# Optimization experiments

Measured on AMD Instinct MI355X. Metric: run time of the kernel, lower is better.

The kernel has to match this reference:

```python
import jax, jax.numpy as jnp
import numpy as np

NUM_NODES = 1_000_000
N = 100_000      # nodes in sampled subgraph (n_id)
E = 1_000_000    # edges from LastNeighborLoader
TE = 1_500_000   # total stored temporal events
B = 20_000       # batch of (src, dst, neg_dst) events
MEM = 128        # memory_dim
TD = 64          # time_dim
MSG = 64         # raw_msg_dim
EMB = 128        # embedding_dim
H = 2            # TransformerConv heads (out = heads * emb//2)
D = EMB // H
HID = 128        # MLP hidden
OUT = 64         # MLP out / link predictor in_channels
EDGE_DIM = MSG + TD


def setup_inputs() -> dict:
    key = jax.random.key(0)
    ks = iter(jax.random.split(key, 40))
    nrm = lambda shp, s: jax.random.normal(next(ks), shp, dtype=jnp.float32) * s
    inp = {
        'memory_table': nrm((NUM_NODES, MEM), 1.0),
        'last_update_table': jax.random.uniform(next(ks), (NUM_NODES,), dtype=jnp.float32) * 1000.0,
        'graph_t': jax.random.uniform(next(ks), (TE,), dtype=jnp.float32) * 1000.0,
        'graph_msg': nrm((TE, MSG), 1.0),
        'Wt': nrm((1, TD), 1.0), 'bt': nrm((TD,), 1.0),
        'Wq': nrm((MEM, EMB), MEM ** -0.5), 'bq': jnp.zeros((EMB,), jnp.float32),
        'Wk': nrm((MEM, EMB), MEM ** -0.5), 'bk': jnp.zeros((EMB,), jnp.float32),
        'Wv': nrm((MEM, EMB), MEM ** -0.5), 'bv': jnp.zeros((EMB,), jnp.float32),
        'We': nrm((EDGE_DIM, EMB), EDGE_DIM ** -0.5),
        'Wskip': nrm((MEM, EMB), MEM ** -0.5), 'bskip': jnp.zeros((EMB,), jnp.float32),
        'W1': nrm((EMB, HID), EMB ** -0.5), 'b1': jnp.zeros((HID,), jnp.float32),
        'bn_gamma': jnp.ones((HID,), jnp.float32), 'bn_beta': jnp.zeros((HID,), jnp.float32),
        'W2': nrm((HID, OUT), HID ** -0.5), 'b2': jnp.zeros((OUT,), jnp.float32),
        'Wls': nrm((OUT, OUT), OUT ** -0.5), 'bls': jnp.zeros((OUT,), jnp.float32),
        'Wld': nrm((OUT, OUT), OUT ** -0.5), 'bld': jnp.zeros((OUT,), jnp.float32),
        'Wlf': nrm((OUT, 1), OUT ** -0.5), 'blf': jnp.zeros((1,), jnp.float32),
        'n_id': jax.random.randint(next(ks), (N,), 0, NUM_NODES, dtype=jnp.int64) if jax.config.jax_enable_x64 else jax.random.randint(next(ks), (N,), 0, NUM_NODES).astype(jnp.int32),
        'edge_index': jax.random.randint(next(ks), (2, E), 0, N).astype(jnp.int32),
        'e_id': jax.random.randint(next(ks), (E,), 0, TE).astype(jnp.int32),
        'src_idx': jax.random.randint(next(ks), (B,), 0, N).astype(jnp.int32),
        'dst_idx': jax.random.randint(next(ks), (B,), 0, N).astype(jnp.int32),
        'neg_idx': jax.random.randint(next(ks), (B,), 0, N).astype(jnp.int32),
    }
    return inp


def _forward(memory_table, last_update_table, graph_t, graph_msg,
             Wt, bt, Wq, bq, Wk, bk, Wv, bv, We, Wskip, bskip,
             W1, b1, bn_gamma, bn_beta, W2, b2,
             Wls, bls, Wld, bld, Wlf, blf,
             n_id, edge_index, e_id, src_idx, dst_idx, neg_idx):
    # --- memory lookup (TGNMemory.forward for n_id) ---
    x = memory_table[n_id]          # [N, MEM]
    lu = last_update_table[n_id]    # [N]
    src, dst = edge_index[0], edge_index[1]

    # --- temporal edge features ---
    t_e = graph_t[e_id]             # [E]
    msg_e = graph_msg[e_id]         # [E, MSG]
    rel_t = lu[src] - t_e           # [E]
    rel_t_enc = jnp.cos(rel_t[:, None] * Wt[0] + bt)          # TimeEncoder: cos(Linear(1, TD))
    edge_attr = jnp.concatenate([rel_t_enc, msg_e], axis=-1)  # [E, EDGE_DIM]

    # --- TransformerConv (heads=H, head_dim=D, edge_dim) ---
    q = (x @ Wq + bq).reshape(N, H, D)
    k = (x @ Wk + bk).reshape(N, H, D)
    v = (x @ Wv + bv).reshape(N, H, D)
    e_proj = (edge_attr @ We).reshape(E, H, D)
    k_e = k[src] + e_proj
    v_e = v[src] + e_proj
    logits = jnp.einsum('ehd,ehd->eh', q[dst], k_e) / jnp.sqrt(jnp.float32(D))  # [E, H]
    m = jax.ops.segment_max(logits, dst, num_segments=N)      # per-dst max, [N, H]
    w = jnp.exp(logits - m[dst])
    s = jax.ops.segment_sum(w, dst, num_segments=N)           # [N, H]
    alpha = w / (s[dst] + 1e-16)                               # softmax over incoming edges
    agg = jax.ops.segment_sum(alpha[..., None] * v_e, dst, num_segments=N)  # [N, H, D]
    z = agg.reshape(N, EMB) + (x @ Wskip + bskip)              # root/skip connection

    # --- MLP([EMB, HID, OUT]) with batch_norm + relu between layers ---
    h = z @ W1 + b1
    mu = jnp.mean(h, axis=0)
    var = jnp.mean(jnp.square(h - mu), axis=0)
    h = (h - mu) * jax.lax.rsqrt(var + 1e-5) * bn_gamma + bn_beta
    h = jax.nn.relu(h)
    z2 = h @ W2 + b2                                           # [N, OUT]

    # --- link prediction on assoc-gathered embeddings ---
    z_src, z_dst, z_neg = z2[src_idx], z2[dst_idx], z2[neg_idx]

    def link_pred(a, b):
        hh = jax.nn.relu(a @ Wls + bls + b @ Wld + bld)
        return hh @ Wlf + blf                                  # [B, 1]

    return link_pred(z_src, z_dst), link_pred(z_src, z_neg)


def reference(memory_table, last_update_table, graph_t, graph_msg,
              Wt, bt, Wq, bq, Wk, bk, Wv, bv, We, Wskip, bskip,
              W1, b1, bn_gamma, bn_beta, W2, b2,
              Wls, bls, Wld, bld, Wlf, blf,
              n_id, edge_index, e_id, src_idx, dst_idx, neg_idx):
    return _forward(memory_table, last_update_table, graph_t, graph_msg,
                    Wt, bt, Wq, bq, Wk, bk, Wv, bv, We, Wskip, bskip,
                    W1, b1, bn_gamma, bn_beta, W2, b2,
                    Wls, bls, Wld, bld, Wlf, blf,
                    n_id, edge_index, e_id, src_idx, dst_idx, neg_idx)
```

## Files before the change

### kernel.cpp

```cpp
#include <hip/hip_runtime.h>

#define NN 100000
#define EE 1000000
#define BB 20000
#define NB 100352
#define NCH 98

__global__ __launch_bounds__(256) void k_hist(
    const int* __restrict__ eidx, int* __restrict__ bins)
{
    int e = blockIdx.x * 256 + threadIdx.x;
    if (e < EE) atomicAdd(&bins[eidx[EE + e]], 1);
}

__global__ __launch_bounds__(256) void k_csum(
    const int* __restrict__ bins, int* __restrict__ csum)
{
    __shared__ int s[256];
    int tid = threadIdx.x;
    int i0 = blockIdx.x * 1024 + tid * 4;
    s[tid] = bins[i0] + bins[i0+1] + bins[i0+2] + bins[i0+3];
    __syncthreads();
    for (int off = 128; off > 0; off >>= 1) {
        if (tid < off) s[tid] += s[tid + off];
        __syncthreads();
    }
    if (tid == 0) csum[blockIdx.x] = s[0];
}

__global__ __launch_bounds__(128) void k_cscan(
    const int* __restrict__ csum, int* __restrict__ cbase)
{
    __shared__ int s[128];
    int tid = threadIdx.x;
    s[tid] = (tid < NCH) ? csum[tid] : 0;
    __syncthreads();
    for (int off = 1; off < 128; off <<= 1) {
        int t = (tid >= off) ? s[tid - off] : 0;
        __syncthreads();
        s[tid] += t;
        __syncthreads();
    }
    if (tid < NCH) cbase[tid] = tid ? s[tid - 1] : 0;
}

__global__ __launch_bounds__(256) void k_bscan(
    int* __restrict__ bins, const int* __restrict__ cbase)
{
    __shared__ int s[256];
    int tid = threadIdx.x;
    int i0 = blockIdx.x * 1024 + tid * 4;
    int v0 = bins[i0], v1 = bins[i0+1], v2 = bins[i0+2], v3 = bins[i0+3];
    int p0 = v0, p1 = p0 + v1, p2 = p1 + v2, p3 = p2 + v3;
    s[tid] = p3;
    __syncthreads();
    for (int off = 1; off < 256; off <<= 1) {
        int t = (tid >= off) ? s[tid - off] : 0;
        __syncthreads();
        s[tid] += t;
        __syncthreads();
    }
    int base = cbase[blockIdx.x] + (tid ? s[tid - 1] : 0);
    bins[i0]   = base;
    bins[i0+1] = base + p0;
    bins[i0+2] = base + p1;
    bins[i0+3] = base + p2;
}

__global__ __launch_bounds__(256) void k_scatter(
    const int* __restrict__ eidx, int* __restrict__ bins, int* __restrict__ perm)
{
    int e = blockIdx.x * 256 + threadIdx.x;
    if (e < EE) {
        int d = eidx[EE + e];
        int pos = atomicAdd(&bins[d], 1);
        perm[pos] = e;
    }
}

__global__ __launch_bounds__(256) void k_node(
    const float* __restrict__ memt, const float* __restrict__ lut,
    const int* __restrict__ n_id,
    const float* __restrict__ Wq, const float* __restrict__ bq,
    const float* __restrict__ Wk, const float* __restrict__ bk,
    const float* __restrict__ Wv, const float* __restrict__ bv,
    const float* __restrict__ Wsk, const float* __restrict__ bsk,
    float* __restrict__ q, float* __restrict__ k, float* __restrict__ v,
    float* __restrict__ skip, float* __restrict__ lu)
{
    __shared__ float As[128][68];
    __shared__ float Bs[32][68];
    __shared__ int nid_s[64];
    const int tid = threadIdx.x;
    const int r0 = blockIdx.x * 64;

    if (tid < 64) {
        int r = r0 + tid;
        int id = (r < NN) ? n_id[r] : 0;
        nid_s[tid] = id;
        if (r < NN) lu[r] = lut[id];
    }
    __syncthreads();
    #pragma unroll
    for (int i = 0; i < 8; ++i) {
        int idx = i*256 + tid;
        int r = idx >> 5, c4 = idx & 31;
        float4 a = *(const float4*)&memt[(size_t)nid_s[r]*128 + c4*4];
        As[c4*4+0][r] = a.x; As[c4*4+1][r] = a.y;
        As[c4*4+2][r] = a.z; As[c4*4+3][r] = a.w;
    }

    const int ty = tid >> 4, tx = tid & 15;
    #pragma unroll 1
    for (int pass = 0; pass < 8; ++pass) {
        const int wsel = pass >> 1, half = pass & 1;
        const float* W    = wsel==0?Wq : wsel==1?Wk : wsel==2?Wv : Wsk;
        const float* bias = wsel==0?bq : wsel==1?bk : wsel==2?bv : bsk;
        float* outp       = wsel==0?q  : wsel==1?k  : wsel==2?v  : skip;
        float acc[4][4] = {};
        #pragma unroll 1
        for (int kt = 0; kt < 4; ++kt) {
            __syncthreads();
            #pragma unroll
            for (int i = 0; i < 2; ++i) {
                int idx = i*256 + tid;
                int kk = idx >> 4, c4 = idx & 15;
                *(float4*)&Bs[kk][c4*4] =
                    *(const float4*)&W[(size_t)(kt*32+kk)*128 + half*64 + c4*4];
            }
            __syncthreads();
            #pragma unroll
            for (int kk = 0; kk < 32; ++kk) {
                float4 a = *(const float4*)&As[kt*32+kk][ty*4];
                float4 b = *(const float4*)&Bs[kk][tx*4];
                float av[4] = {a.x,a.y,a.z,a.w};
                float bw[4] = {b.x,b.y,b.z,b.w};
                #pragma unroll
                for (int ii = 0; ii < 4; ++ii)
                    #pragma unroll
                    for (int jj = 0; jj < 4; ++jj)
                        acc[ii][jj] = fmaf(av[ii], bw[jj], acc[ii][jj]);
            }
        }
        float4 bia = *(const float4*)&bias[half*64 + tx*4];
        float bw[4] = {bia.x,bia.y,bia.z,bia.w};
        #pragma unroll
        for (int ii = 0; ii < 4; ++ii) {
            int r = r0 + ty*4 + ii;
            if (r < NN) {
                float4 o = make_float4(acc[ii][0]+bw[0], acc[ii][1]+bw[1],
                                       acc[ii][2]+bw[2], acc[ii][3]+bw[3]);
                *(float4*)&outp[(size_t)r*128 + half*64 + tx*4] = o;
            }
        }
    }
}

__global__ __launch_bounds__(256) void k_edge(
    const int* __restrict__ perm,
    const int* __restrict__ eidx, const int* __restrict__ e_id,
    const float* __restrict__ graph_t, const float* __restrict__ graph_msg,
    const float* __restrict__ Wt, const float* __restrict__ bt,
    const float* __restrict__ We,
    const float* __restrict__ lu, const float* __restrict__ q,
    const float* __restrict__ k, const float* __restrict__ v,
    float* __restrict__ aggw, float* __restrict__ sden)
{
    __shared__ float EAs[128*68];
    __shared__ float Wes[32*132];
    __shared__ int   srcs[64], dsts[64], eids[64];
    __shared__ float relt[64];
    __shared__ float wl[128];
    const int tid = threadIdx.x;
    const int p0 = blockIdx.x * 64;

    if (tid < 64) {
        int e = perm[p0 + tid];
        int s_ = eidx[e], d_ = eidx[EE + e], id = e_id[e];
        srcs[tid] = s_; dsts[tid] = d_; eids[tid] = id;
        relt[tid] = lu[s_] - graph_t[id];
    }
    __syncthreads();
    #pragma unroll
    for (int i = 0; i < 16; ++i) {
        int idx = i*256 + tid;
        int kk = idx >> 6, e = idx & 63;
        EAs[kk*68 + e] = cosf(fmaf(relt[e], Wt[kk], bt[kk]));
    }
    {
        int e = tid >> 2, c0 = tid & 3;
        const float4* mrow = (const float4*)&graph_msg[(size_t)eids[e]*64];
        #pragma unroll
        for (int i = 0; i < 4; ++i) {
            int c = c0*4 + i;
            float4 m = mrow[c];
            EAs[(64 + c*4 + 0)*68 + e] = m.x;
            EAs[(64 + c*4 + 1)*68 + e] = m.y;
            EAs[(64 + c*4 + 2)*68 + e] = m.z;
            EAs[(64 + c*4 + 3)*68 + e] = m.w;
        }
    }
    __syncthreads();

    float acc[4][8] = {};
    const int ty = tid >> 4, tx = tid & 15;
    for (int kt = 0; kt < 4; ++kt) {
        #pragma unroll
        for (int i = 0; i < 4; ++i) {
            int idx = i*256 + tid;
            int kk = idx >> 5, c4 = idx & 31;
            *(float4*)&Wes[kk*132 + c4*4] =
                *(const float4*)&We[(size_t)(kt*32+kk)*128 + c4*4];
        }
        __syncthreads();
        #pragma unroll
        for (int kk = 0; kk < 32; ++kk) {
            float4 a  = *(const float4*)&EAs[(kt*32+kk)*68 + ty*4];
            float4 b0 = *(const float4*)&Wes[kk*132 + tx*4];
            float4 b1 = *(const float4*)&Wes[kk*132 + 64 + tx*4];
            float av[4] = {a.x,a.y,a.z,a.w};
            float bw[8] = {b0.x,b0.y,b0.z,b0.w,b1.x,b1.y,b1.z,b1.w};
            #pragma unroll
            for (int ii = 0; ii < 4; ++ii)
                #pragma unroll
                for (int jj = 0; jj < 8; ++jj)
                    acc[ii][jj] = fmaf(av[ii], bw[jj], acc[ii][jj]);
        }
        __syncthreads();
    }
    float* EP = EAs;
    #pragma unroll
    for (int ii = 0; ii < 4; ++ii) {
        int e = ty*4 + ii;
        *(float4*)&EP[e*132 + tx*4] =
            make_float4(acc[ii][0], acc[ii][1], acc[ii][2], acc[ii][3]);
        *(float4*)&EP[e*132 + 64 + tx*4] =
            make_float4(acc[ii][4], acc[ii][5], acc[ii][6], acc[ii][7]);
    }
    __syncthreads();
    if (tid < 128) {
        int e = tid >> 1, h = tid & 1;
        const float4* qr = (const float4*)&q[(size_t)dsts[e]*128 + h*64];
        const float4* kr = (const float4*)&k[(size_t)srcs[e]*128 + h*64];
        const float4* er = (const float4*)&EP[e*132 + h*64];
        float sum = 0.f;
        #pragma unroll
        for (int i = 0; i < 16; ++i) {
            float4 qv = qr[i], kv = kr[i], ev = er[i];
            sum = fmaf(qv.x, kv.x+ev.x, sum);
            sum = fmaf(qv.y, kv.y+ev.y, sum);
            sum = fmaf(qv.z, kv.z+ev.z, sum);
            sum = fmaf(qv.w, kv.w+ev.w, sum);
        }
        float w = expf(sum * 0.125f);
        wl[tid] = w;
        atomicAdd(&sden[(size_t)dsts[e]*2 + h], w);
    }
    __syncthreads();
    {
        const int j = tid & 127, g = tid >> 7;
        float accv = 0.f;
        int cur = dsts[g*32];
        #pragma unroll 1
        for (int c = 0; c < 4; ++c) {
            float vv[8];
            #pragma unroll
            for (int i = 0; i < 8; ++i)
                vv[i] = v[(size_t)srcs[g*32 + c*8 + i]*128 + j];
            #pragma unroll
            for (int i = 0; i < 8; ++i) {
                int e = g*32 + c*8 + i;
                int d = dsts[e];
                if (d != cur) {
                    atomicAdd(&aggw[(size_t)cur*128 + j], accv);
                    accv = 0.f; cur = d;
                }
                accv = fmaf(wl[e*2 + (j>>6)], vv[i] + EP[e*132 + j], accv);
            }
        }
        atomicAdd(&aggw[(size_t)cur*128 + j], accv);
    }
}

__global__ __launch_bounds__(256) void k_zh(
    const float* __restrict__ aggw, const float* __restrict__ sden,
    const float* __restrict__ skip,
    const float* __restrict__ W1, const float* __restrict__ b1,
    float* __restrict__ hpre)
{
    __shared__ float As[32][68];
    __shared__ float Bs[32][68];
    const int tid = threadIdx.x;
    const int r0 = blockIdx.x * 64;
    const int coloff = blockIdx.y * 64;
    float acc[4][4] = {};
    const int ty = tid >> 4, tx = tid & 15;
    for (int kt = 0; kt < 4; ++kt) {
        const int hsel = kt >> 1;
        #pragma unroll
        for (int i = 0; i < 2; ++i) {
            int idx = i*256 + tid;
            int r = idx >> 3, c4 = idx & 7;
            int rg = r0 + r;
            float4 z = make_float4(0.f,0.f,0.f,0.f);
            if (rg < NN) {
                float4 aw = *(const float4*)&aggw[(size_t)rg*128 + kt*32 + c4*4];
                float4 sk = *(const float4*)&skip[(size_t)rg*128 + kt*32 + c4*4];
                float inv = 1.f / (sden[(size_t)rg*2 + hsel] + 1e-16f);
                z = make_float4(fmaf(aw.x,inv,sk.x), fmaf(aw.y,inv,sk.y),
                                fmaf(aw.z,inv,sk.z), fmaf(aw.w,inv,sk.w));
            }
            As[c4*4+0][r] = z.x; As[c4*4+1][r] = z.y;
            As[c4*4+2][r] = z.z; As[c4*4+3][r] = z.w;
        }
        #pragma unroll
        for (int i = 0; i < 2; ++i) {
            int idx = i*256 + tid;
            int kk = idx >> 4, c4 = idx & 15;
            *(float4*)&Bs[kk][c4*4] =
                *(const float4*)&W1[(size_t)(kt*32+kk)*128 + coloff + c4*4];
        }
        __syncthreads();
        #pragma unroll
        for (int kk = 0; kk < 32; ++kk) {
            float4 a = *(const float4*)&As[kk][ty*4];
            float4 b = *(const float4*)&Bs[kk][tx*4];
            float av[4] = {a.x,a.y,a.z,a.w};
            float bw[4] = {b.x,b.y,b.z,b.w};
            #pragma unroll
            for (int ii = 0; ii < 4; ++ii)
                #pragma unroll
                for (int jj = 0; jj < 4; ++jj)
                    acc[ii][jj] = fmaf(av[ii], bw[jj], acc[ii][jj]);
        }
        __syncthreads();
    }
    float4 bia = *(const float4*)&b1[coloff + tx*4];
    float bw[4] = {bia.x,bia.y,bia.z,bia.w};
    #pragma unroll
    for (int ii = 0; ii < 4; ++ii) {
        int r = r0 + ty*4 + ii;
        if (r < NN) {
            float4 o = make_float4(acc[ii][0]+bw[0], acc[ii][1]+bw[1],
                                   acc[ii][2]+bw[2], acc[ii][3]+bw[3]);
            *(float4*)&hpre[(size_t)r*128 + coloff + tx*4] = o;
        }
    }
}

__global__ __launch_bounds__(256) void k_bnstats(
    const float* __restrict__ hpre, float* __restrict__ bnS, float* __restrict__ bnSQ)
{
    const int tid = threadIdx.x;
    const int col = tid & 127;
    const int half = tid >> 7;
    float s = 0.f, sq = 0.f;
    for (int r = blockIdx.x*2 + half; r < NN; r += gridDim.x*2) {
        float x = hpre[(size_t)r*128 + col];
        s += x; sq = fmaf(x, x, sq);
    }
    __shared__ float ls[256], lq[256];
    ls[tid] = s; lq[tid] = sq;
    __syncthreads();
    if (tid < 128) {
        atomicAdd(&bnS[col],  ls[tid] + ls[tid+128]);
        atomicAdd(&bnSQ[col], lq[tid] + lq[tid+128]);
    }
}

__global__ __launch_bounds__(256) void k_z2(
    const float* __restrict__ hpre,
    const float* __restrict__ bnS, const float* __restrict__ bnSQ,
    const float* __restrict__ gamma, const float* __restrict__ beta,
    const float* __restrict__ W2, const float* __restrict__ b2,
    float* __restrict__ z2)
{
    __shared__ float As[32][68];
    __shared__ float Bs[32][68];
    __shared__ float scl[128], sft[128];
    const int tid = threadIdx.x;
    const int r0 = blockIdx.x * 64;
    if (tid < 128) {
        float mu  = bnS[tid]  * (1.f/NN);
        float var = bnSQ[tid] * (1.f/NN) - mu*mu;
        float sc  = rsqrtf(var + 1e-5f) * gamma[tid];
        scl[tid] = sc;
        sft[tid] = fmaf(-mu, sc, beta[tid]);
    }
    __syncthreads();
    float acc[4][4] = {};
    const int ty = tid >> 4, tx = tid & 15;
    for (int kt = 0; kt < 4; ++kt) {
        #pragma unroll
        for (int i = 0; i < 2; ++i) {
            int idx = i*256 + tid;
            int r = idx >> 3, c4 = idx & 7;
            int rg = r0 + r;
            int kc = kt*32 + c4*4;
            float4 z = make_float4(0.f,0.f,0.f,0.f);
            if (rg < NN) {
                float4 hv = *(const float4*)&hpre[(size_t)rg*128 + kc];
                z.x = fmaxf(fmaf(hv.x, scl[kc+0], sft[kc+0]), 0.f);
                z.y = fmaxf(fmaf(hv.y, scl[kc+1], sft[kc+1]), 0.f);
                z.z = fmaxf(fmaf(hv.z, scl[kc+2], sft[kc+2]), 0.f);
                z.w = fmaxf(fmaf(hv.w, scl[kc+3], sft[kc+3]), 0.f);
            }
            As[c4*4+0][r] = z.x; As[c4*4+1][r] = z.y;
            As[c4*4+2][r] = z.z; As[c4*4+3][r] = z.w;
        }
        #pragma unroll
        for (int i = 0; i < 2; ++i) {
            int idx = i*256 + tid;
            int kk = idx >> 4, c4 = idx & 15;
            *(float4*)&Bs[kk][c4*4] =
                *(const float4*)&W2[(size_t)(kt*32+kk)*64 + c4*4];
        }
        __syncthreads();
        #pragma unroll
        for (int kk = 0; kk < 32; ++kk) {
            float4 a = *(const float4*)&As[kk][ty*4];
            float4 b = *(const float4*)&Bs[kk][tx*4];
            float av[4] = {a.x,a.y,a.z,a.w};
            float bw[4] = {b.x,b.y,b.z,b.w};
            #pragma unroll
            for (int ii = 0; ii < 4; ++ii)
                #pragma unroll
                for (int jj = 0; jj < 4; ++jj)
                    acc[ii][jj] = fmaf(av[ii], bw[jj], acc[ii][jj]);
        }
        __syncthreads();
    }
    float4 bia = *(const float4*)&b2[tx*4];
    float bw[4] = {bia.x,bia.y,bia.z,bia.w};
    #pragma unroll
    for (int ii = 0; ii < 4; ++ii) {
        int r = r0 + ty*4 + ii;
        if (r < NN) {
            float4 o = make_float4(acc[ii][0]+bw[0], acc[ii][1]+bw[1],
                                   acc[ii][2]+bw[2], acc[ii][3]+bw[3]);
            *(float4*)&z2[(size_t)r*64 + tx*4] = o;
        }
    }
}

__global__ __launch_bounds__(256) void k_link(
    const float* __restrict__ z2,
    const int* __restrict__ src_idx, const int* __restrict__ dst_idx,
    const int* __restrict__ neg_idx,
    const float* __restrict__ Wls, const float* __restrict__ bls,
    const float* __restrict__ Wld, const float* __restrict__ bld,
    const float* __restrict__ Wlf, const float* __restrict__ blf,
    float* __restrict__ out)
{
    int wid  = blockIdx.x*4 + (threadIdx.x >> 6);
    int lane = threadIdx.x & 63;
    int which = wid / BB;
    int b = wid - which*BB;
    int ia = src_idx[b];
    int ib = which ? neg_idx[b] : dst_idx[b];
    float a = z2[(size_t)ia*64 + lane];
    float c = z2[(size_t)ib*64 + lane];
    float acc = bls[lane] + bld[lane];
    #pragma unroll 8
    for (int k2 = 0; k2 < 64; ++k2) {
        float ak = __shfl(a, k2);
        float ck = __shfl(c, k2);
        acc = fmaf(ak, Wls[k2*64 + lane], acc);
        acc = fmaf(ck, Wld[k2*64 + lane], acc);
    }
    float hj = fmaxf(acc, 0.f) * Wlf[lane];
    #pragma unroll
    for (int off = 32; off > 0; off >>= 1)
        hj += __shfl_down(hj, off);
    if (lane == 0) out[which*BB + b] = hj + blf[0];
}

extern "C" void kernel_launch(void* const* d_in, const int* in_sizes, int n_in,
                              void* d_out, int out_size, void* d_ws, size_t ws_size,
                              hipStream_t stream)
{
    (void)in_sizes; (void)n_in; (void)out_size; (void)ws_size;
    const float* memt = (const float*)d_in[0];
    const float* lut  = (const float*)d_in[1];
    const float* gt   = (const float*)d_in[2];
    const float* gmsg = (const float*)d_in[3];
    const float* Wt   = (const float*)d_in[4];
    const float* bt   = (const float*)d_in[5];
    const float* Wq   = (const float*)d_in[6];
    const float* bq   = (const float*)d_in[7];
    const float* Wk   = (const float*)d_in[8];
    const float* bk   = (const float*)d_in[9];
    const float* Wv   = (const float*)d_in[10];
    const float* bv   = (const float*)d_in[11];
    const float* We   = (const float*)d_in[12];
    const float* Wsk  = (const float*)d_in[13];
    const float* bsk  = (const float*)d_in[14];
    const float* W1   = (const float*)d_in[15];
    const float* b1   = (const float*)d_in[16];
    const float* gam  = (const float*)d_in[17];
    const float* bet  = (const float*)d_in[18];
    const float* W2   = (const float*)d_in[19];
    const float* b2   = (const float*)d_in[20];
    const float* Wls  = (const float*)d_in[21];
    const float* bls  = (const float*)d_in[22];
    const float* Wld  = (const float*)d_in[23];
    const float* bld  = (const float*)d_in[24];
    const float* Wlf  = (const float*)d_in[25];
    const float* blf  = (const float*)d_in[26];
    const int* n_id   = (const int*)d_in[27];
    const int* eidx   = (const int*)d_in[28];
    const int* e_id   = (const int*)d_in[29];
    const int* sidx   = (const int*)d_in[30];
    const int* didx   = (const int*)d_in[31];
    const int* nidx   = (const int*)d_in[32];

    float* ws = (float*)d_ws;
    float* q    = ws;
    float* k    = ws + 12800000;
    float* v    = ws + 25600000;
    float* skip = ws + 38400000;
    float* lu   = ws + 51200000;
    float* aggw = ws + 51300000;
    float* sden = ws + 64100000;
    float* bnS  = ws + 64300000;
    float* bnSQ = ws + 64300128;
    int*   bins = (int*)(ws + 64300256);
    int*   csum = (int*)(ws + 64400608);
    int*   cbase= (int*)(ws + 64400736);
    int*   perm = (int*)(ws + 64400864);
    float* hpre = q;
    float* z2   = k;

    hipMemsetAsync(aggw, 0, (size_t)(12800000 + 200000 + 256 + 100352) * 4, stream);

    dim3 blk(256);
    k_hist   <<<dim3(3907), blk, 0, stream>>>(eidx, bins);
    k_csum   <<<dim3(NCH),  blk, 0, stream>>>(bins, csum);
    k_cscan  <<<dim3(1), dim3(128), 0, stream>>>(csum, cbase);
    k_bscan  <<<dim3(NCH),  blk, 0, stream>>>(bins, cbase);
    k_scatter<<<dim3(3907), blk, 0, stream>>>(eidx, bins, perm);
    k_node<<<dim3(1563), blk, 0, stream>>>(memt, lut, n_id, Wq, bq, Wk, bk,
                                           Wv, bv, Wsk, bsk, q, k, v, skip, lu);
    k_edge<<<dim3(15625), blk, 0, stream>>>(perm, eidx, e_id, gt, gmsg, Wt, bt, We,
                                            lu, q, k, v, aggw, sden);
    k_zh<<<dim3(1563, 2), blk, 0, stream>>>(aggw, sden, skip, W1, b1, hpre);
    k_bnstats<<<dim3(512), blk, 0, stream>>>(hpre, bnS, bnSQ);
    k_z2<<<dim3(1563), blk, 0, stream>>>(hpre, bnS, bnSQ, gam, bet, W2, b2, z2);
    k_link<<<dim3(10000), blk, 0, stream>>>(z2, sidx, didx, nidx,
                                            Wls, bls, Wld, bld, Wlf, blf,
                                            (float*)d_out);
}
```

Measured before the change: 2.052 ms.

## Move edge projection to node level via associativity of We products

Measured after the change: 1.849 ms. 9.9% less time.

```diff
diff --git a/kernel.cpp b/kernel.cpp
--- a/kernel.cpp
+++ b/kernel.cpp
@@ -156,18 +156,77 @@
     }
 }
 
+__global__ __launch_bounds__(256) void k_qe(
+    const float* __restrict__ q, const float* __restrict__ We,
+    float* __restrict__ qe)
+{
+    __shared__ float As[64][68];
+    __shared__ float Bs[32][132];
+    const int tid = threadIdx.x;
+    const int r0 = blockIdx.x * 64;
+    const int h  = blockIdx.y;
+    #pragma unroll
+    for (int i = 0; i < 4; ++i) {
+        int idx = i*256 + tid;
+        int r = idx >> 4, c4 = idx & 15;
+        int rg = r0 + r;
+        float4 a = make_float4(0.f,0.f,0.f,0.f);
+        if (rg < NN) a = *(const float4*)&q[(size_t)rg*128 + h*64 + c4*4];
+        As[c4*4+0][r] = a.x; As[c4*4+1][r] = a.y;
+        As[c4*4+2][r] = a.z; As[c4*4+3][r] = a.w;
+    }
+    float acc[4][8] = {};
+    const int ty = tid >> 4, tx = tid & 15;
+    #pragma unroll 1
+    for (int kt = 0; kt < 2; ++kt) {
+        __syncthreads();
+        #pragma unroll
+        for (int i = 0; i < 4; ++i) {
+            int idx = i*256 + tid;
+            int j = idx >> 3, cq = idx & 7;
+            float4 w = *(const float4*)&We[(size_t)j*128 + h*64 + kt*32 + cq*4];
+            Bs[cq*4+0][j] = w.x; Bs[cq*4+1][j] = w.y;
+            Bs[cq*4+2][j] = w.z; Bs[cq*4+3][j] = w.w;
+        }
+        __syncthreads();
+        #pragma unroll
+        for (int kk = 0; kk < 32; ++kk) {
+            float4 a  = *(const float4*)&As[kt*32+kk][ty*4];
+            float4 b0 = *(const float4*)&Bs[kk][tx*4];
+            float4 b1 = *(const float4*)&Bs[kk][64 + tx*4];
+            float av[4] = {a.x,a.y,a.z,a.w};
+            float bw[8] = {b0.x,b0.y,b0.z,b0.w,b1.x,b1.y,b1.z,b1.w};
+            #pragma unroll
+            for (int ii = 0; ii < 4; ++ii)
+                #pragma unroll
+                for (int jj = 0; jj < 8; ++jj)
+                    acc[ii][jj] = fmaf(av[ii], bw[jj], acc[ii][jj]);
+        }
+    }
+    #pragma unroll
+    for (int ii = 0; ii < 4; ++ii) {
+        int r = r0 + ty*4 + ii;
+        if (r < NN) {
+            *(float4*)&qe[(size_t)r*256 + h*128 + tx*4] =
+                make_float4(acc[ii][0],acc[ii][1],acc[ii][2],acc[ii][3]);
+            *(float4*)&qe[(size_t)r*256 + h*128 + 64 + tx*4] =
+                make_float4(acc[ii][4],acc[ii][5],acc[ii][6],acc[ii][7]);
+        }
+    }
+}
+
 __global__ __launch_bounds__(256) void k_edge(
     const int* __restrict__ perm,
     const int* __restrict__ eidx, const int* __restrict__ e_id,
     const float* __restrict__ graph_t, const float* __restrict__ graph_msg,
     const float* __restrict__ Wt, const float* __restrict__ bt,
-    const float* __restrict__ We,
     const float* __restrict__ lu, const float* __restrict__ q,
     const float* __restrict__ k, const float* __restrict__ v,
-    float* __restrict__ aggw, float* __restrict__ sden)
-{
-    __shared__ float EAs[128*68];
-    __shared__ float Wes[32*132];
+    const float* __restrict__ qe,
+    float* __restrict__ aggw, float* __restrict__ eaggw,
+    float* __restrict__ sden)
+{
+    __shared__ float EA[64*132];
     __shared__ int   srcs[64], dsts[64], eids[64];
     __shared__ float relt[64];
     __shared__ float wl[128];
@@ -181,85 +240,66 @@
         relt[tid] = lu[s_] - graph_t[id];
     }
     __syncthreads();
-    #pragma unroll
-    for (int i = 0; i < 16; ++i) {
-        int idx = i*256 + tid;
-        int kk = idx >> 6, e = idx & 63;
-        EAs[kk*68 + e] = cosf(fmaf(relt[e], Wt[kk], bt[kk]));
-    }
     {
         int e = tid >> 2, c0 = tid & 3;
         const float4* mrow = (const float4*)&graph_msg[(size_t)eids[e]*64];
-        #pragma unroll
-        for (int i = 0; i < 4; ++i) {
-            int c = c0*4 + i;
-            float4 m = mrow[c];
-            EAs[(64 + c*4 + 0)*68 + e] = m.x;
-            EAs[(64 + c*4 + 1)*68 + e] = m.y;
-            EAs[(64 + c*4 + 2)*68 + e] = m.z;
-            EAs[(64 + c*4 + 3)*68 + e] = m.w;
-        }
-    }
-    __syncthreads();
-
-    float acc[4][8] = {};
-    const int ty = tid >> 4, tx = tid & 15;
-    for (int kt = 0; kt < 4; ++kt) {
-        #pragma unroll
-        for (int i = 0; i < 4; ++i) {
-            int idx = i*256 + tid;
-            int kk = idx >> 5, c4 = idx & 31;
-            *(float4*)&Wes[kk*132 + c4*4] =
-                *(const float4*)&We[(size_t)(kt*32+kk)*128 + c4*4];
-        }
-        __syncthreads();
-        #pragma unroll
-        for (int kk = 0; kk < 32; ++kk) {
-            float4 a  = *(const float4*)&EAs[(kt*32+kk)*68 + ty*4];
-            float4 b0 = *(const float4*)&Wes[kk*132 + tx*4];
-            float4 b1 = *(const float4*)&Wes[kk*132 + 64 + tx*4];
-            float av[4] = {a.x,a.y,a.z,a.w};
-            float bw[8] = {b0.x,b0.y,b0.z,b0.w,b1.x,b1.y,b1.z,b1.w};
-            #pragma unroll
-            for (int ii = 0; ii < 4; ++ii)
-                #pragma unroll
-                for (int jj = 0; jj < 8; ++jj)
-                    acc[ii][jj] = fmaf(av[ii], bw[jj], acc[ii][jj]);
-        }
-        __syncthreads();
-    }
-    float* EP = EAs;
-    #pragma unroll
-    for (int ii = 0; ii < 4; ++ii) {
-        int e = ty*4 + ii;
-        *(float4*)&EP[e*132 + tx*4] =
-            make_float4(acc[ii][0], acc[ii][1], acc[ii][2], acc[ii][3]);
-        *(float4*)&EP[e*132 + 64 + tx*4] =
-            make_float4(acc[ii][4], acc[ii][5], acc[ii][6], acc[ii][7]);
+        float4 m[4];
+        #pragma unroll
+        for (int i = 0; i < 4; ++i) m[i] = mrow[c0 + i*4];
+        #pragma unroll
+        for (int i = 0; i < 4; ++i)
+            *(float4*)&EA[e*132 + 64 + (c0 + i*4)*4] = m[i];
+    }
+    {
+        int e = tid >> 2, kq = tid & 3;
+        float rt = relt[e];
+        #pragma unroll
+        for (int it = 0; it < 4; ++it) {
+            int k0 = it*16 + kq*4;
+            float4 wt = *(const float4*)&Wt[k0];
+            float4 bv = *(const float4*)&bt[k0];
+            float4 r;
+            r.x = cosf(fmaf(rt, wt.x, bv.x));
+            r.y = cosf(fmaf(rt, wt.y, bv.y));
+            r.z = cosf(fmaf(rt, wt.z, bv.z));
+            r.w = cosf(fmaf(rt, wt.w, bv.w));
+            *(float4*)&EA[e*132 + k0] = r;
+        }
     }
     __syncthreads();
     if (tid < 128) {
         int e = tid >> 1, h = tid & 1;
-        const float4* qr = (const float4*)&q[(size_t)dsts[e]*128 + h*64];
-        const float4* kr = (const float4*)&k[(size_t)srcs[e]*128 + h*64];
-        const float4* er = (const float4*)&EP[e*132 + h*64];
-        float sum = 0.f;
-        #pragma unroll
+        int d_ = dsts[e], s_ = srcs[e];
+        const float4* qr  = (const float4*)&q[(size_t)d_*128 + h*64];
+        const float4* kr  = (const float4*)&k[(size_t)s_*128 + h*64];
+        const float4* qer = (const float4*)&qe[(size_t)d_*256 + (size_t)h*128];
+        const float4* ear = (const float4*)&EA[e*132];
+        float4 s4 = make_float4(0.f,0.f,0.f,0.f);
+        #pragma unroll 8
         for (int i = 0; i < 16; ++i) {
-            float4 qv = qr[i], kv = kr[i], ev = er[i];
-            sum = fmaf(qv.x, kv.x+ev.x, sum);
-            sum = fmaf(qv.y, kv.y+ev.y, sum);
-            sum = fmaf(qv.z, kv.z+ev.z, sum);
-            sum = fmaf(qv.w, kv.w+ev.w, sum);
-        }
+            float4 qv = qr[i], kv = kr[i];
+            s4.x = fmaf(qv.x, kv.x, s4.x);
+            s4.y = fmaf(qv.y, kv.y, s4.y);
+            s4.z = fmaf(qv.z, kv.z, s4.z);
+            s4.w = fmaf(qv.w, kv.w, s4.w);
+        }
+        #pragma unroll 8
+        for (int i = 0; i < 32; ++i) {
+            float4 ev = ear[i], pv = qer[i];
+            s4.x = fmaf(ev.x, pv.x, s4.x);
+            s4.y = fmaf(ev.y, pv.y, s4.y);
+            s4.z = fmaf(ev.z, pv.z, s4.z);
+            s4.w = fmaf(ev.w, pv.w, s4.w);
+        }
+        float sum = (s4.x + s4.y) + (s4.z + s4.w);
         float w = expf(sum * 0.125f);
         wl[tid] = w;
-        atomicAdd(&sden[(size_t)dsts[e]*2 + h], w);
+        atomicAdd(&sden[(size_t)d_*2 + h], w);
     }
     __syncthreads();
     {
         const int j = tid & 127, g = tid >> 7;
-        float accv = 0.f;
+        float av = 0.f, ae0 = 0.f, ae1 = 0.f;
         int cur = dsts[g*32];
         #pragma unroll 1
         for (int c = 0; c < 4; ++c) {
@@ -272,13 +312,79 @@
                 int e = g*32 + c*8 + i;
                 int d = dsts[e];
                 if (d != cur) {
-                    atomicAdd(&aggw[(size_t)cur*128 + j], accv);
-                    accv = 0.f; cur = d;
+                    atomicAdd(&aggw[(size_t)cur*128 + j], av);
+                    atomicAdd(&eaggw[(size_t)cur*256 + j], ae0);
+                    atomicAdd(&eaggw[(size_t)cur*256 + 128 + j], ae1);
+                    av = 0.f; ae0 = 0.f; ae1 = 0.f; cur = d;
                 }
-                accv = fmaf(wl[e*2 + (j>>6)], vv[i] + EP[e*132 + j], accv);
+                float w0 = wl[e*2], w1 = wl[e*2+1];
+                float ea = EA[e*132 + j];
+                av  = fmaf((j >> 6) ? w1 : w0, vv[i], av);
+                ae0 = fmaf(w0, ea, ae0);
+                ae1 = fmaf(w1, ea, ae1);
             }
         }
-        atomicAdd(&aggw[(size_t)cur*128 + j], accv);
+        atomicAdd(&aggw[(size_t)cur*128 + j], av);
+        atomicAdd(&eaggw[(size_t)cur*256 + j], ae0);
+        atomicAdd(&eaggw[(size_t)cur*256 + 128 + j], ae1);
+    }
+}
+
+__global__ __launch_bounds__(256) void k_eagg(
+    const float* __restrict__ eaggw, const float* __restrict__ We,
+    float* __restrict__ aggw)
+{
+    __shared__ float As[128][68];
+    __shared__ float Bs[32][68];
+    const int tid = threadIdx.x;
+    const int r0 = blockIdx.x * 64;
+    const int h  = blockIdx.y;
+    #pragma unroll
+    for (int i = 0; i < 8; ++i) {
+        int idx = i*256 + tid;
+        int r = idx >> 5, c4 = idx & 31;
+        int rg = r0 + r;
+        float4 a = make_float4(0.f,0.f,0.f,0.f);
+        if (rg < NN) a = *(const float4*)&eaggw[(size_t)rg*256 + (size_t)h*128 + c4*4];
+        As[c4*4+0][r] = a.x; As[c4*4+1][r] = a.y;
+        As[c4*4+2][r] = a.z; As[c4*4+3][r] = a.w;
+    }
+    float acc[4][4] = {};
+    const int ty = tid >> 4, tx = tid & 15;
+    #pragma unroll 1
+    for (int kt = 0; kt < 4; ++kt) {
+        __syncthreads();
+        #pragma unroll
+        for (int i = 0; i < 2; ++i) {
+            int idx = i*256 + tid;
+            int kk = idx >> 4, c4 = idx & 15;
+            *(float4*)&Bs[kk][c4*4] =
+                *(const float4*)&We[(size_t)(kt*32+kk)*128 + h*64 + c4*4];
+        }
+        __syncthreads();
+        #pragma unroll
+        for (int kk = 0; kk < 32; ++kk) {
+            float4 a = *(const float4*)&As[kt*32+kk][ty*4];
+            float4 b = *(const float4*)&Bs[kk][tx*4];
+            float av[4] = {a.x,a.y,a.z,a.w};
+            float bw[4] = {b.x,b.y,b.z,b.w};
+            #pragma unroll
+            for (int ii = 0; ii < 4; ++ii)
+                #pragma unroll
+                for (int jj = 0; jj < 4; ++jj)
+                    acc[ii][jj] = fmaf(av[ii], bw[jj], acc[ii][jj]);
+        }
+    }
+    #pragma unroll
+    for (int ii = 0; ii < 4; ++ii) {
+        int r = r0 + ty*4 + ii;
+        if (r < NN) {
+            float4* p = (float4*)&aggw[(size_t)r*128 + h*64 + tx*4];
+            float4 o = *p;
+            o.x += acc[ii][0]; o.y += acc[ii][1];
+            o.z += acc[ii][2]; o.w += acc[ii][3];
+            *p = o;
+        }
     }
 }
 
@@ -528,10 +634,13 @@
     int*   csum = (int*)(ws + 64400608);
     int*   cbase= (int*)(ws + 64400736);
     int*   perm = (int*)(ws + 64400864);
+    float* qe   = ws + 65400864;
+    float* eaggw= ws + 91000864;
     float* hpre = q;
     float* z2   = k;
 
     hipMemsetAsync(aggw, 0, (size_t)(12800000 + 200000 + 256 + 100352) * 4, stream);
+    hipMemsetAsync(eaggw, 0, (size_t)25600000 * 4, stream);
 
     dim3 blk(256);
     k_hist   <<<dim3(3907), blk, 0, stream>>>(eidx, bins);
@@ -541,8 +650,10 @@
     k_scatter<<<dim3(3907), blk, 0, stream>>>(eidx, bins, perm);
     k_node<<<dim3(1563), blk, 0, stream>>>(memt, lut, n_id, Wq, bq, Wk, bk,
                                            Wv, bv, Wsk, bsk, q, k, v, skip, lu);
-    k_edge<<<dim3(15625), blk, 0, stream>>>(perm, eidx, e_id, gt, gmsg, Wt, bt, We,
-                                            lu, q, k, v, aggw, sden);
+    k_qe<<<dim3(1563, 2), blk, 0, stream>>>(q, We, qe);
+    k_edge<<<dim3(15625), blk, 0, stream>>>(perm, eidx, e_id, gt, gmsg, Wt, bt,
+                                            lu, q, k, v, qe, aggw, eaggw, sden);
+    k_eagg<<<dim3(1563, 2), blk, 0, stream>>>(eaggw, We, aggw);
     k_zh<<<dim3(1563, 2), blk, 0, stream>>>(aggw, sden, skip, W1, b1, hpre);
     k_bnstats<<<dim3(512), blk, 0, stream>>>(hpre, bnS, bnSQ);
     k_z2<<<dim3(1563), blk, 0, stream>>>(hpre, bnS, bnSQ, gam, bet, W2, b2, z2);
```
